# Kernel tuning notes

Measured on AMD Instinct MI355X. Metric: run time of the kernel, lower is better.

The kernel has to match this reference:

```python
import jax, jax.numpy as jnp
import numpy as np
from jax import lax

IN_CH = 256
NUM_CLASSES = 21
ROI = 7
SCALE = 1.0 / 32
SR = 2  # sampling_ratio
B = 2
NPROP = 128
FH = FW = 32
IMG = 1024
SCORE_THRESH = 0.05
NMS_THRESH = 0.5
MAX_DET = 100


def setup_inputs() -> dict:
    key = jax.random.key(0)
    ks = jax.random.split(key, 10)
    features = jax.random.normal(ks[0], (B, IN_CH, FH, FW), jnp.float32)
    x1 = jax.random.uniform(ks[1], (B, NPROP), minval=0.0, maxval=IMG - 160.0)
    y1 = jax.random.uniform(ks[2], (B, NPROP), minval=0.0, maxval=IMG - 160.0)
    w = jax.random.uniform(ks[3], (B, NPROP), minval=32.0, maxval=160.0)
    h = jax.random.uniform(ks[4], (B, NPROP), minval=32.0, maxval=160.0)
    proposals = jnp.stack([x1, y1, x1 + w, y1 + h], axis=-1)  # [B, NPROP, 4]
    img_sizes = jnp.full((B, 2), IMG, dtype=jnp.int32)  # (h, w)
    feat_dim = IN_CH * ROI * ROI

    def kaiming(k, shape):
        return jax.random.normal(k, shape, jnp.float32) * np.float32(np.sqrt(2.0 / shape[1]))

    W1 = kaiming(ks[5], (1024, feat_dim)); b1 = jnp.zeros((1024,), jnp.float32)
    W2 = kaiming(ks[6], (1024, 1024)); b2 = jnp.zeros((1024,), jnp.float32)
    Wc = jax.random.normal(ks[7], (NUM_CLASSES, 1024), jnp.float32) * 0.01
    bc = jnp.zeros((NUM_CLASSES,), jnp.float32)
    Wb = jax.random.normal(ks[8], (NUM_CLASSES * 4, 1024), jnp.float32) * 0.001
    bb = jnp.zeros((NUM_CLASSES * 4,), jnp.float32)
    return dict(features=features, proposals=proposals, img_sizes=img_sizes,
                W1=W1, b1=b1, W2=W2, b2=b2, Wc=Wc, bc=bc, Wb=Wb, bb=bb)


def roi_align(features, bidx, rois):
    """torchvision-style RoIAlign (aligned=False), spatial_scale=SCALE, sampling_ratio=SR.
    features [B,C,H,W], bidx [N] int, rois [N,4] -> [N, C*ROI*ROI] (channel-major flatten)."""
    Bf, C, H, W = features.shape
    x1 = rois[:, 0] * SCALE; y1 = rois[:, 1] * SCALE
    x2 = rois[:, 2] * SCALE; y2 = rois[:, 3] * SCALE
    rw = jnp.maximum(x2 - x1, 1.0); rh = jnp.maximum(y2 - y1, 1.0)
    bw = rw / ROI; bh = rh / ROI
    # per-bin sample offsets: [ROI, SR]
    g = jnp.arange(ROI, dtype=jnp.float32)[:, None] + (jnp.arange(SR, dtype=jnp.float32)[None, :] + 0.5) / SR
    ys = y1[:, None, None] + g[None] * bh[:, None, None]  # [N, ROI, SR]
    xs = x1[:, None, None] + g[None] * bw[:, None, None]  # [N, ROI, SR]
    y = ys[:, :, :, None, None]  # [N,ph,sy,1,1]
    x = xs[:, None, None, :, :]  # [N,1,1,pw,sx]
    inb = (y >= -1.0) & (y <= H) & (x >= -1.0) & (x <= W)  # [N,ph,sy,pw,sx]
    yc = jnp.clip(y, 0.0, H - 1.0); xc = jnp.clip(x, 0.0, W - 1.0)
    y0f = jnp.floor(yc); x0f = jnp.floor(xc)
    y0 = y0f.astype(jnp.int32); x0 = x0f.astype(jnp.int32)
    y1i = jnp.minimum(y0 + 1, H - 1); x1i = jnp.minimum(x0 + 1, W - 1)
    ly = yc - y0f; lx = xc - x0f
    hy = 1.0 - ly; hx = 1.0 - lx
    b = bidx[:, None, None, None, None]
    # gather four corners: advanced indices broadcast -> [N,ph,sy,pw,sx,C]
    f00 = features[b, :, y0, x0]
    f01 = features[b, :, y0, x1i]
    f10 = features[b, :, y1i, x0]
    f11 = features[b, :, y1i, x1i]
    val = ((hy * hx)[..., None] * f00 + (hy * lx)[..., None] * f01
           + (ly * hx)[..., None] * f10 + (ly * lx)[..., None] * f11)
    val = val * inb[..., None]
    pooled = val.mean(axis=(2, 4))            # [N, ph, pw, C]
    pooled = jnp.transpose(pooled, (0, 3, 1, 2))  # [N, C, ph, pw] (torch layout)
    return pooled.reshape(pooled.shape[0], -1)


def decode_boxes(deltas, props):
    pw = props[..., 2] - props[..., 0]
    ph = props[..., 3] - props[..., 1]
    px = props[..., 0] + pw / 2
    py = props[..., 1] + ph / 2
    cx = px + deltas[..., 0] * pw
    cy = py + deltas[..., 1] * ph
    w = pw * jnp.exp(deltas[..., 2])
    h = ph * jnp.exp(deltas[..., 3])
    return jnp.stack([cx - w / 2, cy - h / 2, cx + w / 2, cy + h / 2], axis=-1)


def nms_fixed(boxes, scores, valid, iou_thresh, max_out):
    """Greedy NMS with fixed shapes. Returns (indices[max_out], ok_mask[max_out])."""
    M = scores.shape[0]
    s = jnp.where(valid, scores, -jnp.inf)
    order = jnp.argsort(-s)
    b = boxes[order]; v = valid[order]
    bx1, by1, bx2, by2 = b[:, 0], b[:, 1], b[:, 2], b[:, 3]
    area = (bx2 - bx1) * (by2 - by1)
    idxs = jnp.arange(M)

    def body(i, keep):
        xi1 = jnp.maximum(bx1[i], bx1); yi1 = jnp.maximum(by1[i], by1)
        xi2 = jnp.minimum(bx2[i], bx2); yi2 = jnp.minimum(by2[i], by2)
        inter = jnp.maximum(xi2 - xi1, 0.0) * jnp.maximum(yi2 - yi1, 0.0)
        iou = inter / (area[i] + area - inter + 1e-9)
        suppress = (iou > iou_thresh) & (idxs > i)
        return jnp.where(keep[i], keep & ~suppress, keep)

    keep = lax.fori_loop(0, M, body, v)
    pos = jnp.where(keep, idxs, M)
    take = jnp.sort(pos)[:max_out]
    ok = take < M
    take = jnp.where(ok, take, 0)
    return order[take], ok


def postprocess_image(probs, reg, props, img_hw):
    Ncls = probs.shape[1]
    scores = probs[:, 1:]                    # [N, C-1] (skip background)
    deltas = reg[:, 1:, :]                   # [N, C-1, 4]
    boxes = decode_boxes(deltas, props[:, None, :])  # [N, C-1, 4]
    h = img_hw[0].astype(boxes.dtype); w = img_hw[1].astype(boxes.dtype)
    boxes = jnp.stack([jnp.clip(boxes[..., 0], 0.0, w), jnp.clip(boxes[..., 1], 0.0, h),
                       jnp.clip(boxes[..., 2], 0.0, w), jnp.clip(boxes[..., 3], 0.0, h)], axis=-1)
    labels = jnp.broadcast_to(jnp.arange(1, Ncls, dtype=jnp.int32)[None, :], scores.shape)
    fb = boxes.reshape(-1, 4); fs = scores.reshape(-1); fl = labels.reshape(-1)
    valid = fs > SCORE_THRESH
    maxc = jnp.max(jnp.where(valid, jnp.max(fb, axis=1), 0.0))
    off = fl.astype(fb.dtype) * (maxc + 1.0)
    zero = jnp.zeros_like(off)
    fb_off = fb + jnp.stack([off, zero, off, zero], axis=-1)
    idx, ok = nms_fixed(fb_off, fs, valid, NMS_THRESH, MAX_DET)
    m = ok.astype(fb.dtype)
    return fb[idx] * m[:, None], fs[idx] * m, fl[idx] * ok.astype(jnp.int32)


def reference(features, proposals, img_sizes, W1, b1, W2, b2, Wc, bc, Wb, bb):
    Bn, NP = proposals.shape[0], proposals.shape[1]
    bidx = jnp.repeat(jnp.arange(Bn, dtype=jnp.int32), NP)
    props_flat = proposals.reshape(-1, 4)
    roi_feats = roi_align(features, bidx, props_flat)       # [N, C*49]
    x = jax.nn.relu(roi_feats @ W1.T + b1)
    x = jax.nn.relu(x @ W2.T + b2)
    cls_logits = x @ Wc.T + bc                              # [N, NUM_CLASSES]
    box_reg = (x @ Wb.T + bb).reshape(-1, NUM_CLASSES, 4)   # [N, NUM_CLASSES, 4]
    probs = jax.nn.softmax(cls_logits, axis=-1)
    out_b, out_s, out_l = [], [], []
    for i in range(Bn):
        p = probs[i * NP:(i + 1) * NP]
        r = box_reg[i * NP:(i + 1) * NP]
        bi, si, li = postprocess_image(p, r, proposals[i], img_sizes[i])
        out_b.append(bi); out_s.append(si); out_l.append(li)
    return jnp.stack(out_b), jnp.stack(out_s), jnp.stack(out_l)
```

## Files before the change

### kernel.cpp

```cpp
#include <hip/hip_runtime.h>
#include <math.h>

#define IN_CH   256
#define NCLS    21
#define ROIW    7
#define NPROP   128
#define BATCH   2
#define NROI    (BATCH*NPROP)
#define FEAT_DIM (IN_CH*ROIW*ROIW)
#define HID     1024
#define NCAND   (NPROP*(NCLS-1))
#define MAXDET  100
#define SCORE_T 0.05f
#define NMS_T   0.5f

__global__ __launch_bounds__(256) void transpose_feat(const float* __restrict__ feat,
                                                      float* __restrict__ ft) {
    int img = blockIdx.z;
    int cb = blockIdx.y;
    int pb = blockIdx.x;
    __shared__ float t[32][33];
    int tx = threadIdx.x & 31, ty = threadIdx.x >> 5;
#pragma unroll
    for (int i = 0; i < 4; ++i) {
        int c = ty + i * 8;
        t[c][tx] = feat[(size_t)img * 262144 + (size_t)(cb * 32 + c) * 1024 + pb * 32 + tx];
    }
    __syncthreads();
#pragma unroll
    for (int i = 0; i < 4; ++i) {
        int p = ty + i * 8;
        ft[(size_t)img * 262144 + (size_t)(pb * 32 + p) * 256 + cb * 32 + tx] = t[tx][p];
    }
}

__global__ __launch_bounds__(256) void roi_align_tr(const float* __restrict__ ft,
                                                    const float* __restrict__ props,
                                                    float* __restrict__ out) {
    int n = blockIdx.x >> 1;
    int half = blockIdx.x & 1;
    int img = n / NPROP;
    int q0 = half ? 25 : 0;
    int nq = half ? 24 : 25;
    const float* pr = props + n * 4;
    float x1 = pr[0] * 0.03125f, y1 = pr[1] * 0.03125f;
    float x2 = pr[2] * 0.03125f, y2 = pr[3] * 0.03125f;
    float rw = fmaxf(x2 - x1, 1.0f), rh = fmaxf(y2 - y1, 1.0f);
    float bw = rw / 7.0f, bh = rh / 7.0f;
    int cg = threadIdx.x & 63;
    int qg = threadIdx.x >> 6;
    __shared__ float tile[25][260];
    const float* base = ft + (size_t)img * 262144 + cg * 4;
    for (int j = qg; j < nq; j += 4) {
        int q = q0 + j;
        int iy = q / 7, ix = q % 7;
        float ax = 0.f, ay = 0.f, az = 0.f, aw = 0.f;
#pragma unroll
        for (int s = 0; s < 4; ++s) {
            int sy = s >> 1, sx = s & 1;
            float gy = (float)iy + ((float)sy + 0.5f) / 2.0f;
            float gx = (float)ix + ((float)sx + 0.5f) / 2.0f;
            float y = y1 + gy * bh;
            float x = x1 + gx * bw;
            bool inb = (y >= -1.0f) && (y <= 32.0f) && (x >= -1.0f) && (x <= 32.0f);
            float yc = fminf(fmaxf(y, 0.0f), 31.0f);
            float xc = fminf(fmaxf(x, 0.0f), 31.0f);
            float y0f = floorf(yc), x0f = floorf(xc);
            int y0 = (int)y0f, x0i = (int)x0f;
            int y1i = min(y0 + 1, 31), x1i = min(x0i + 1, 31);
            float ly = yc - y0f, lx = xc - x0f;
            float hy = 1.0f - ly, hx = 1.0f - lx;
            float wg = inb ? 1.0f : 0.0f;
            float w00 = hy * hx * wg, w01 = hy * lx * wg, w10 = ly * hx * wg, w11 = ly * lx * wg;
            float4 f00 = *(const float4*)(base + (size_t)(y0 * 32 + x0i) * 256);
            float4 f01 = *(const float4*)(base + (size_t)(y0 * 32 + x1i) * 256);
            float4 f10 = *(const float4*)(base + (size_t)(y1i * 32 + x0i) * 256);
            float4 f11 = *(const float4*)(base + (size_t)(y1i * 32 + x1i) * 256);
            ax += w00 * f00.x + w01 * f01.x + w10 * f10.x + w11 * f11.x;
            ay += w00 * f00.y + w01 * f01.y + w10 * f10.y + w11 * f11.y;
            az += w00 * f00.z + w01 * f01.z + w10 * f10.z + w11 * f11.z;
            aw += w00 * f00.w + w01 * f01.w + w10 * f10.w + w11 * f11.w;
        }
        *(float4*)&tile[j][cg * 4] = make_float4(ax * 0.25f, ay * 0.25f, az * 0.25f, aw * 0.25f);
    }
    __syncthreads();
    float* ob = out + (size_t)n * FEAT_DIM + q0;
    int tid = threadIdx.x;
    if (half == 0) {
        for (int i = tid; i < 256 * 25; i += 256) {
            int c = i / 25, ql = i % 25;
            ob[c * 49 + ql] = tile[ql][c];
        }
    } else {
        for (int i = tid; i < 256 * 24; i += 256) {
            int c = i / 24, ql = i % 24;
            ob[c * 49 + ql] = tile[ql][c];
        }
    }
}

#define GBM 128
#define GBN 128
#define GBK 16
__global__ __launch_bounds__(256) void gemm_tn_part(const float* __restrict__ A,
                                                    const float* __restrict__ Wt,
                                                    float* __restrict__ Cp,
                                                    int Nr, int Mo, int K) {
    const int S = gridDim.z;
    const int kchunk = K / S;
    const int k0 = blockIdx.z * kchunk;
    const int n0 = blockIdx.y * GBM;
    const int j0 = blockIdx.x * GBN;
    __shared__ float As[GBK][GBM + 4];
    __shared__ float Ws[GBK][GBN + 4];
    const int tid = threadIdx.x;
    const int tx = tid & 15;
    const int ty = tid >> 4;
    const int r0 = tx << 2;
    const int c0 = ty << 2;
    const int srow = tid >> 1;
    const int skk = (tid & 1) << 3;
    float acc[8][8];
#pragma unroll
    for (int r = 0; r < 8; ++r)
#pragma unroll
        for (int c = 0; c < 8; ++c) acc[r][c] = 0.0f;

    const int iters = kchunk / GBK;
    const float* Abase = A + (size_t)(n0 + srow) * K + skk;
    const float* Wbase = Wt + (size_t)(j0 + srow) * K + skk;
    float4 pa0 = *(const float4*)(Abase + k0);
    float4 pa1 = *(const float4*)(Abase + k0 + 4);
    float4 pw0 = *(const float4*)(Wbase + k0);
    float4 pw1 = *(const float4*)(Wbase + k0 + 4);

#pragma unroll 1
    for (int it = 0; it < iters; ++it) {
        __syncthreads();
        As[skk + 0][srow] = pa0.x; As[skk + 1][srow] = pa0.y; As[skk + 2][srow] = pa0.z; As[skk + 3][srow] = pa0.w;
        As[skk + 4][srow] = pa1.x; As[skk + 5][srow] = pa1.y; As[skk + 6][srow] = pa1.z; As[skk + 7][srow] = pa1.w;
        Ws[skk + 0][srow] = pw0.x; Ws[skk + 1][srow] = pw0.y; Ws[skk + 2][srow] = pw0.z; Ws[skk + 3][srow] = pw0.w;
        Ws[skk + 4][srow] = pw1.x; Ws[skk + 5][srow] = pw1.y; Ws[skk + 6][srow] = pw1.z; Ws[skk + 7][srow] = pw1.w;
        __syncthreads();
        if (it + 1 < iters) {
            int kc = k0 + (it + 1) * GBK;
            pa0 = *(const float4*)(Abase + kc);
            pa1 = *(const float4*)(Abase + kc + 4);
            pw0 = *(const float4*)(Wbase + kc);
            pw1 = *(const float4*)(Wbase + kc + 4);
        }
        float4 fa0[2], fa1[2], fw0[2], fw1[2];
        fa0[0] = *(const float4*)&As[0][r0];
        fa1[0] = *(const float4*)&As[0][r0 + 64];
        fw0[0] = *(const float4*)&Ws[0][c0];
        fw1[0] = *(const float4*)&Ws[0][c0 + 64];
#pragma unroll
        for (int k = 0; k < GBK; ++k) {
            const int cur = k & 1, nxt = cur ^ 1;
            if (k + 1 < GBK) {
                fa0[nxt] = *(const float4*)&As[k + 1][r0];
                fa1[nxt] = *(const float4*)&As[k + 1][r0 + 64];
                fw0[nxt] = *(const float4*)&Ws[k + 1][c0];
                fw1[nxt] = *(const float4*)&Ws[k + 1][c0 + 64];
            }
            float a[8] = {fa0[cur].x, fa0[cur].y, fa0[cur].z, fa0[cur].w,
                          fa1[cur].x, fa1[cur].y, fa1[cur].z, fa1[cur].w};
            float w[8] = {fw0[cur].x, fw0[cur].y, fw0[cur].z, fw0[cur].w,
                          fw1[cur].x, fw1[cur].y, fw1[cur].z, fw1[cur].w};
#pragma unroll
            for (int r = 0; r < 8; ++r)
#pragma unroll
                for (int c = 0; c < 8; ++c)
                    acc[r][c] = fmaf(a[r], w[c], acc[r][c]);
        }
    }
#pragma unroll
    for (int r = 0; r < 8; ++r) {
        int gr = n0 + ((r < 4) ? (r0 + r) : (r0 + 64 + r - 4));
        float* o = Cp + ((size_t)blockIdx.z * Nr + gr) * Mo + j0;
        *(float4*)(o + c0)      = make_float4(acc[r][0], acc[r][1], acc[r][2], acc[r][3]);
        *(float4*)(o + c0 + 64) = make_float4(acc[r][4], acc[r][5], acc[r][6], acc[r][7]);
    }
}

__global__ __launch_bounds__(256) void reduce_bias_relu(const float* __restrict__ Cp,
                                                        const float* __restrict__ bias,
                                                        float* __restrict__ X,
                                                        int Nr, int Mo, int S) {
    int idx = blockIdx.x * 256 + threadIdx.x;
    int total = (Nr * Mo) >> 2;
    if (idx >= total) return;
    int e = idx << 2;
    int j = e % Mo;
    float4 s = make_float4(0.f, 0.f, 0.f, 0.f);
    for (int ss = 0; ss < S; ++ss) {
        float4 c = *(const float4*)(Cp + (size_t)ss * Nr * Mo + e);
        s.x += c.x; s.y += c.y; s.z += c.z; s.w += c.w;
    }
    float4 b = *(const float4*)(bias + j);
    s.x = fmaxf(s.x + b.x, 0.f); s.y = fmaxf(s.y + b.y, 0.f);
    s.z = fmaxf(s.z + b.z, 0.f); s.w = fmaxf(s.w + b.w, 0.f);
    *(float4*)(X + e) = s;
}

__global__ __launch_bounds__(256) void heads_cand_k(const float* __restrict__ Cp2,
                                                    const float* __restrict__ b2,
                                                    const float* __restrict__ Wc, const float* __restrict__ bc,
                                                    const float* __restrict__ Wb, const float* __restrict__ bb,
                                                    const float* __restrict__ props,
                                                    const int* __restrict__ img_sizes,
                                                    float* __restrict__ cbox,
                                                    float* __restrict__ csc,
                                                    unsigned long long* __restrict__ ckey,
                                                    int* __restrict__ vcount) {
    int n = blockIdx.x;
    int tid = threadIdx.x;
    if (n == 0 && tid < 2) vcount[tid] = 0;
    __shared__ float xs[HID];
    __shared__ float lg[NCLS];
    __shared__ float bs[84];
    __shared__ float ssum;
    {
        int e = n * HID + tid * 4;
        float4 s = make_float4(0.f, 0.f, 0.f, 0.f);
#pragma unroll
        for (int ss = 0; ss < 16; ++ss) {
            float4 c = *(const float4*)(Cp2 + (size_t)ss * (NROI * HID) + e);
            s.x += c.x; s.y += c.y; s.z += c.z; s.w += c.w;
        }
        float4 b = *(const float4*)(b2 + tid * 4);
        s.x = fmaxf(s.x + b.x, 0.f); s.y = fmaxf(s.y + b.y, 0.f);
        s.z = fmaxf(s.z + b.z, 0.f); s.w = fmaxf(s.w + b.w, 0.f);
        *(float4*)&xs[tid * 4] = s;
    }
    __syncthreads();
    int wave = tid >> 6, lane = tid & 63;
    for (int h = wave; h < 105; h += 4) {
        const float* w = (h < 21) ? (Wc + (size_t)h * HID) : (Wb + (size_t)(h - 21) * HID);
        float acc = 0.0f;
#pragma unroll
        for (int k0 = 0; k0 < HID; k0 += 256) {
            float4 wv = *(const float4*)(w + k0 + lane * 4);
            float4 xv = *(const float4*)&xs[k0 + lane * 4];
            acc = fmaf(wv.x, xv.x, acc);
            acc = fmaf(wv.y, xv.y, acc);
            acc = fmaf(wv.z, xv.z, acc);
            acc = fmaf(wv.w, xv.w, acc);
        }
#pragma unroll
        for (int m = 32; m; m >>= 1) acc += __shfl_xor(acc, m, 64);
        if (lane == 0) {
            if (h < 21) lg[h] = acc + bc[h];
            else bs[h - 21] = acc + bb[h - 21];
        }
    }
    __syncthreads();
    if (tid == 0) {
        float m = lg[0];
        for (int c = 1; c < 21; ++c) m = fmaxf(m, lg[c]);
        float s = 0.0f;
        for (int c = 0; c < 21; ++c) { float e = expf(lg[c] - m); lg[c] = e; s += e; }
        ssum = s;
    }
    __syncthreads();
    if (tid < 20) {
        int c = tid + 1;
        int img = n / NPROP;
        float s = lg[c] / ssum;
        const float* pr = props + n * 4;
        float pw = pr[2] - pr[0], ph = pr[3] - pr[1];
        float px = pr[0] + pw * 0.5f, py = pr[1] + ph * 0.5f;
        const float* d = &bs[c * 4];
        float cx = px + d[0] * pw;
        float cy = py + d[1] * ph;
        float w = pw * expf(d[2]);
        float h = ph * expf(d[3]);
        float bx1 = cx - w * 0.5f, by1 = cy - h * 0.5f, bx2 = cx + w * 0.5f, by2 = cy + h * 0.5f;
        float Wi = (float)img_sizes[img * 2 + 1], Hi = (float)img_sizes[img * 2 + 0];
        bx1 = fminf(fmaxf(bx1, 0.f), Wi); by1 = fminf(fmaxf(by1, 0.f), Hi);
        bx2 = fminf(fmaxf(bx2, 0.f), Wi); by2 = fminf(fmaxf(by2, 0.f), Hi);
        int t = n * 20 + tid;
        *(float4*)(cbox + (size_t)t * 4) = make_float4(bx1, by1, bx2, by2);
        csc[t] = s;
        bool valid = s > SCORE_T;
        unsigned int sb = __float_as_uint(s);
        int m = t - img * NCAND;
        ckey[t] = valid ? (((unsigned long long)sb << 32) | (unsigned int)(NCAND - 1 - m)) : 0ull;
    }
}

__global__ __launch_bounds__(256) void rank_k(const float* __restrict__ cbox,
                                              const float* __restrict__ csc,
                                              const unsigned long long* __restrict__ ckey,
                                              float* __restrict__ sbox, float* __restrict__ ssc,
                                              int* __restrict__ sm, int* __restrict__ vcount) {
    int img = blockIdx.x / 40;
    int seg = blockIdx.x % 40;
    int base = img * NCAND;
    int lm = threadIdx.x & 63;
    int chunk = threadIdx.x >> 6;
    int m = seg * 64 + lm;
    __shared__ __align__(16) unsigned long long keys[NCAND];
    for (int j = threadIdx.x; j < NCAND; j += 256) keys[j] = ckey[base + j];
    unsigned long long mykey = ckey[base + m];
    float s = csc[base + m];
    bool valid = s > SCORE_T;
    __syncthreads();
    const ulonglong2* kp = (const ulonglong2*)&keys[chunk * 640];
    int r = 0;
#pragma unroll 4
    for (int j = 0; j < 320; ++j) {
        ulonglong2 kk = kp[j];
        r += (kk.x > mykey) ? 1 : 0;
        r += (kk.y > mykey) ? 1 : 0;
    }
    __shared__ int part[4][64];
    part[chunk][lm] = r;
    __syncthreads();
    if (chunk == 0) {
        int rank = part[0][lm] + part[1][lm] + part[2][lm] + part[3][lm];
        if (valid) {
            int o = base + rank;
            *(float4*)(sbox + (size_t)o * 4) = *(const float4*)(cbox + (size_t)(base + m) * 4);
            ssc[o] = s;
            sm[o] = m;
        }
    }
    int cnt = __syncthreads_count((chunk == 0) && valid);
    if (threadIdx.x == 0) atomicAdd(&vcount[img], cnt);
}

__global__ __launch_bounds__(64) void nms_k(const int* __restrict__ sm,
                                            const float* __restrict__ sbox,
                                            const int* __restrict__ vcount,
                                            int* __restrict__ skeep) {
    int bid = blockIdx.x;
    int img = bid / 20;
    int cls = bid % 20 + 1;
    int V = vcount[img];
    __shared__ float lx1[128], ly1[128], lx2[128], ly2[128];
    __shared__ int lpos[128];
    __shared__ int lcnt;
    __shared__ int keepL[128];
    int lane = threadIdx.x;
    if (lane == 0) lcnt = 0;
    __syncthreads();
    for (int p0 = 0; p0 < V; p0 += 64) {
        int p = p0 + lane;
        bool pred = false;
        if (p < V) {
            int m = sm[img * NCAND + p];
            pred = (m % 20 + 1) == cls;
        }
        unsigned long long mask = __ballot(pred);
        int base = lcnt;
        if (pred) {
            int idx = base + __popcll(mask & ((1ull << lane) - 1ull));
            const float* bx = sbox + (size_t)(img * NCAND + (p0 + lane)) * 4;
            lx1[idx] = bx[0]; ly1[idx] = bx[1]; lx2[idx] = bx[2]; ly2[idx] = bx[3];
            lpos[idx] = p0 + lane;
        }
        __syncthreads();
        if (lane == 0) lcnt += (int)__popcll(mask);
        __syncthreads();
    }
    int C = lcnt;
    for (int j = lane; j < 128; j += 64) keepL[j] = 1;
    __syncthreads();
    for (int i = 0; i < C; ++i) {
        __syncthreads();
        if (keepL[i] == 0) continue;
        float X1 = lx1[i], Y1 = ly1[i], X2 = lx2[i], Y2 = ly2[i];
        float ai = (X2 - X1) * (Y2 - Y1);
        for (int j = i + 1 + lane; j < C; j += 64) {
            if (keepL[j]) {
                float xi1 = fmaxf(X1, lx1[j]);
                float yi1 = fmaxf(Y1, ly1[j]);
                float xi2 = fminf(X2, lx2[j]);
                float yi2 = fminf(Y2, ly2[j]);
                float inter = fmaxf(xi2 - xi1, 0.f) * fmaxf(yi2 - yi1, 0.f);
                float aj = (lx2[j] - lx1[j]) * (ly2[j] - ly1[j]);
                float iou = inter / (ai + aj - inter + 1e-9f);
                if (iou > NMS_T) keepL[j] = 0;
            }
        }
    }
    __syncthreads();
    for (int j = lane; j < C; j += 64) skeep[img * NCAND + lpos[j]] = keepL[j];
}

__global__ __launch_bounds__(256) void write_k(const float* __restrict__ sbox,
                                               const float* __restrict__ ssc,
                                               const int* __restrict__ sm,
                                               const int* __restrict__ skeep,
                                               const int* __restrict__ vcount,
                                               float* __restrict__ out) {
    int img = blockIdx.x;
    int tid = threadIdx.x;
    float* ob = out + img * MAXDET * 4;
    float* os = out + BATCH * MAXDET * 4 + img * MAXDET;
    float* ol = out + BATCH * MAXDET * 5 + img * MAXDET;
    for (int i = tid; i < MAXDET * 4; i += 256) ob[i] = 0.0f;
    for (int i = tid; i < MAXDET; i += 256) { os[i] = 0.0f; ol[i] = 0.0f; }
    __syncthreads();
    int V = vcount[img];
    int chunk = (V + 255) / 256;
    int lo = tid * chunk, hi = min(lo + chunk, V);
    int cnt = 0;
    for (int p = lo; p < hi; ++p) cnt += skeep[img * NCAND + p];
    __shared__ int cs[256];
    __shared__ int pre[256];
    cs[tid] = cnt;
    __syncthreads();
    if (tid == 0) {
        int run = 0;
        for (int t = 0; t < 256; ++t) { pre[t] = run; run += cs[t]; }
    }
    __syncthreads();
    int r = pre[tid];
    for (int p = lo; p < hi; ++p) {
        if (skeep[img * NCAND + p]) {
            if (r < MAXDET) {
                const float* bx = sbox + (size_t)(img * NCAND + p) * 4;
                ob[r * 4 + 0] = bx[0]; ob[r * 4 + 1] = bx[1];
                ob[r * 4 + 2] = bx[2]; ob[r * 4 + 3] = bx[3];
                os[r] = ssc[img * NCAND + p];
                ol[r] = (float)(sm[img * NCAND + p] % 20 + 1);
            }
            ++r;
        }
    }
}

extern "C" void kernel_launch(void* const* d_in, const int* in_sizes, int n_in,
                              void* d_out, int out_size, void* d_ws, size_t ws_size,
                              hipStream_t stream) {
    const float* features  = (const float*)d_in[0];
    const float* proposals = (const float*)d_in[1];
    const int*   img_sizes = (const int*)d_in[2];
    const float* W1 = (const float*)d_in[3];
    const float* b1 = (const float*)d_in[4];
    const float* W2 = (const float*)d_in[5];
    const float* b2 = (const float*)d_in[6];
    const float* Wc = (const float*)d_in[7];
    const float* bc = (const float*)d_in[8];
    const float* Wb = (const float*)d_in[9];
    const float* bb = (const float*)d_in[10];
    float* out = (float*)d_out;

    float* ws = (float*)d_ws;
    float* roi   = ws;
    float* x1    = roi + 3211264;
    float* cpart = x1 + 262144;
    float* featT = cpart;
    float* cbox  = cpart + 16 * 262144;
    float* csc   = cbox + 20480;
    unsigned long long* ckey = (unsigned long long*)(csc + 5120);
    float* sbox  = csc + 5120 + 10240;
    float* ssc   = sbox + 20480;
    int*   sm    = (int*)(ssc + 5120);
    int*   skeep = sm + 5120;
    int*   vcnt  = skeep + 5120;

    hipLaunchKernelGGL(transpose_feat, dim3(32, 8, 2), dim3(256), 0, stream, features, featT);
    hipLaunchKernelGGL(roi_align_tr, dim3(NROI * 2), dim3(256), 0, stream, featT, proposals, roi);
    hipLaunchKernelGGL(gemm_tn_part, dim3(8, 2, 16), dim3(256), 0, stream, roi, W1, cpart, NROI, HID, FEAT_DIM);
    hipLaunchKernelGGL(reduce_bias_relu, dim3(256), dim3(256), 0, stream, cpart, b1, x1, NROI, HID, 16);
    hipLaunchKernelGGL(gemm_tn_part, dim3(8, 2, 16), dim3(256), 0, stream, x1, W2, cpart, NROI, HID, HID);
    hipLaunchKernelGGL(heads_cand_k, dim3(NROI), dim3(256), 0, stream, cpart, b2, Wc, bc, Wb, bb,
                       proposals, img_sizes, cbox, csc, ckey, vcnt);
    hipLaunchKernelGGL(rank_k, dim3(80), dim3(256), 0, stream, cbox, csc, ckey, sbox, ssc, sm, vcnt);
    hipLaunchKernelGGL(nms_k, dim3(BATCH * 20), dim3(64), 0, stream, sm, sbox, vcnt, skeep);
    hipLaunchKernelGGL(write_k, dim3(BATCH), dim3(256), 0, stream, sbox, ssc, sm, skeep, vcnt, out);
}
```

Baseline: 319.9 us.

## Fuse detection tail into one cooperative kernel and simplify GEMM LDS loads

Merges the heads/candidate, ranking, NMS and output-writing kernels into a single cooperative kernel separated by grid-wide syncs. This removes several kernel launches and inter-kernel gaps in the post-processing tail. NMS now runs with 256 threads per block instead of 64. Separately, the GEMM inner loop drops its register double-buffering of shared-memory fragments in favour of direct per-k loads, which may reduce register pressure but loses the explicit load/compute overlap. Cooperative launch adds grid-sync overhead and requires all blocks to be co-resident.

```diff
diff --git a/kernel.cpp b/kernel.cpp
--- a/kernel.cpp
+++ b/kernel.cpp
@@ -1,5 +1,8 @@
 #include <hip/hip_runtime.h>
+#include <hip/hip_cooperative_groups.h>
 #include <math.h>
+
+namespace cg = cooperative_groups;
 
 #define IN_CH   256
 #define NCLS    21
@@ -149,24 +152,14 @@
             pw0 = *(const float4*)(Wbase + kc);
             pw1 = *(const float4*)(Wbase + kc + 4);
         }
-        float4 fa0[2], fa1[2], fw0[2], fw1[2];
-        fa0[0] = *(const float4*)&As[0][r0];
-        fa1[0] = *(const float4*)&As[0][r0 + 64];
-        fw0[0] = *(const float4*)&Ws[0][c0];
-        fw1[0] = *(const float4*)&Ws[0][c0 + 64];
 #pragma unroll
         for (int k = 0; k < GBK; ++k) {
-            const int cur = k & 1, nxt = cur ^ 1;
-            if (k + 1 < GBK) {
-                fa0[nxt] = *(const float4*)&As[k + 1][r0];
-                fa1[nxt] = *(const float4*)&As[k + 1][r0 + 64];
-                fw0[nxt] = *(const float4*)&Ws[k + 1][c0];
-                fw1[nxt] = *(const float4*)&Ws[k + 1][c0 + 64];
-            }
-            float a[8] = {fa0[cur].x, fa0[cur].y, fa0[cur].z, fa0[cur].w,
-                          fa1[cur].x, fa1[cur].y, fa1[cur].z, fa1[cur].w};
-            float w[8] = {fw0[cur].x, fw0[cur].y, fw0[cur].z, fw0[cur].w,
-                          fw1[cur].x, fw1[cur].y, fw1[cur].z, fw1[cur].w};
+            float4 t0 = *(const float4*)&As[k][r0];
+            float4 t1 = *(const float4*)&As[k][r0 + 64];
+            float4 u0 = *(const float4*)&Ws[k][c0];
+            float4 u1 = *(const float4*)&Ws[k][c0 + 64];
+            float a[8] = {t0.x, t0.y, t0.z, t0.w, t1.x, t1.y, t1.z, t1.w};
+            float w[8] = {u0.x, u0.y, u0.z, u0.w, u1.x, u1.y, u1.z, u1.w};
 #pragma unroll
             for (int r = 0; r < 8; ++r)
 #pragma unroll
@@ -203,231 +196,224 @@
     *(float4*)(X + e) = s;
 }
 
-__global__ __launch_bounds__(256) void heads_cand_k(const float* __restrict__ Cp2,
-                                                    const float* __restrict__ b2,
-                                                    const float* __restrict__ Wc, const float* __restrict__ bc,
-                                                    const float* __restrict__ Wb, const float* __restrict__ bb,
-                                                    const float* __restrict__ props,
-                                                    const int* __restrict__ img_sizes,
-                                                    float* __restrict__ cbox,
-                                                    float* __restrict__ csc,
-                                                    unsigned long long* __restrict__ ckey,
-                                                    int* __restrict__ vcount) {
-    int n = blockIdx.x;
-    int tid = threadIdx.x;
-    if (n == 0 && tid < 2) vcount[tid] = 0;
+__global__ __launch_bounds__(256) void tail_k(const float* __restrict__ Cp2,
+                                              const float* __restrict__ b2,
+                                              const float* __restrict__ Wc, const float* __restrict__ bc,
+                                              const float* __restrict__ Wb, const float* __restrict__ bb,
+                                              const float* __restrict__ props,
+                                              const int* __restrict__ img_sizes,
+                                              float* __restrict__ cbox,
+                                              float* __restrict__ csc,
+                                              unsigned long long* __restrict__ ckey,
+                                              float* __restrict__ sbox, float* __restrict__ ssc,
+                                              int* __restrict__ sm, int* __restrict__ skeep,
+                                              int* __restrict__ vcount,
+                                              float* __restrict__ out) {
+    cg::grid_group grid = cg::this_grid();
+    const int bid = blockIdx.x;
+    const int tid = threadIdx.x;
+
     __shared__ float xs[HID];
     __shared__ float lg[NCLS];
     __shared__ float bs[84];
     __shared__ float ssum;
-    {
-        int e = n * HID + tid * 4;
-        float4 s = make_float4(0.f, 0.f, 0.f, 0.f);
-#pragma unroll
-        for (int ss = 0; ss < 16; ++ss) {
-            float4 c = *(const float4*)(Cp2 + (size_t)ss * (NROI * HID) + e);
-            s.x += c.x; s.y += c.y; s.z += c.z; s.w += c.w;
-        }
-        float4 b = *(const float4*)(b2 + tid * 4);
-        s.x = fmaxf(s.x + b.x, 0.f); s.y = fmaxf(s.y + b.y, 0.f);
-        s.z = fmaxf(s.z + b.z, 0.f); s.w = fmaxf(s.w + b.w, 0.f);
-        *(float4*)&xs[tid * 4] = s;
-    }
-    __syncthreads();
-    int wave = tid >> 6, lane = tid & 63;
-    for (int h = wave; h < 105; h += 4) {
-        const float* w = (h < 21) ? (Wc + (size_t)h * HID) : (Wb + (size_t)(h - 21) * HID);
-        float acc = 0.0f;
-#pragma unroll
-        for (int k0 = 0; k0 < HID; k0 += 256) {
-            float4 wv = *(const float4*)(w + k0 + lane * 4);
-            float4 xv = *(const float4*)&xs[k0 + lane * 4];
-            acc = fmaf(wv.x, xv.x, acc);
-            acc = fmaf(wv.y, xv.y, acc);
-            acc = fmaf(wv.z, xv.z, acc);
-            acc = fmaf(wv.w, xv.w, acc);
-        }
-#pragma unroll
-        for (int m = 32; m; m >>= 1) acc += __shfl_xor(acc, m, 64);
-        if (lane == 0) {
-            if (h < 21) lg[h] = acc + bc[h];
-            else bs[h - 21] = acc + bb[h - 21];
-        }
-    }
-    __syncthreads();
-    if (tid == 0) {
-        float m = lg[0];
-        for (int c = 1; c < 21; ++c) m = fmaxf(m, lg[c]);
-        float s = 0.0f;
-        for (int c = 0; c < 21; ++c) { float e = expf(lg[c] - m); lg[c] = e; s += e; }
-        ssum = s;
-    }
-    __syncthreads();
-    if (tid < 20) {
-        int c = tid + 1;
-        int img = n / NPROP;
-        float s = lg[c] / ssum;
-        const float* pr = props + n * 4;
-        float pw = pr[2] - pr[0], ph = pr[3] - pr[1];
-        float px = pr[0] + pw * 0.5f, py = pr[1] + ph * 0.5f;
-        const float* d = &bs[c * 4];
-        float cx = px + d[0] * pw;
-        float cy = py + d[1] * ph;
-        float w = pw * expf(d[2]);
-        float h = ph * expf(d[3]);
-        float bx1 = cx - w * 0.5f, by1 = cy - h * 0.5f, bx2 = cx + w * 0.5f, by2 = cy + h * 0.5f;
-        float Wi = (float)img_sizes[img * 2 + 1], Hi = (float)img_sizes[img * 2 + 0];
-        bx1 = fminf(fmaxf(bx1, 0.f), Wi); by1 = fminf(fmaxf(by1, 0.f), Hi);
-        bx2 = fminf(fmaxf(bx2, 0.f), Wi); by2 = fminf(fmaxf(by2, 0.f), Hi);
-        int t = n * 20 + tid;
-        *(float4*)(cbox + (size_t)t * 4) = make_float4(bx1, by1, bx2, by2);
-        csc[t] = s;
-        bool valid = s > SCORE_T;
-        unsigned int sb = __float_as_uint(s);
-        int m = t - img * NCAND;
-        ckey[t] = valid ? (((unsigned long long)sb << 32) | (unsigned int)(NCAND - 1 - m)) : 0ull;
-    }
-}
-
-__global__ __launch_bounds__(256) void rank_k(const float* __restrict__ cbox,
-                                              const float* __restrict__ csc,
-                                              const unsigned long long* __restrict__ ckey,
-                                              float* __restrict__ sbox, float* __restrict__ ssc,
-                                              int* __restrict__ sm, int* __restrict__ vcount) {
-    int img = blockIdx.x / 40;
-    int seg = blockIdx.x % 40;
-    int base = img * NCAND;
-    int lm = threadIdx.x & 63;
-    int chunk = threadIdx.x >> 6;
-    int m = seg * 64 + lm;
     __shared__ __align__(16) unsigned long long keys[NCAND];
-    for (int j = threadIdx.x; j < NCAND; j += 256) keys[j] = ckey[base + j];
-    unsigned long long mykey = ckey[base + m];
-    float s = csc[base + m];
-    bool valid = s > SCORE_T;
-    __syncthreads();
-    const ulonglong2* kp = (const ulonglong2*)&keys[chunk * 640];
-    int r = 0;
-#pragma unroll 4
-    for (int j = 0; j < 320; ++j) {
-        ulonglong2 kk = kp[j];
-        r += (kk.x > mykey) ? 1 : 0;
-        r += (kk.y > mykey) ? 1 : 0;
-    }
     __shared__ int part[4][64];
-    part[chunk][lm] = r;
-    __syncthreads();
-    if (chunk == 0) {
-        int rank = part[0][lm] + part[1][lm] + part[2][lm] + part[3][lm];
-        if (valid) {
-            int o = base + rank;
-            *(float4*)(sbox + (size_t)o * 4) = *(const float4*)(cbox + (size_t)(base + m) * 4);
-            ssc[o] = s;
-            sm[o] = m;
-        }
-    }
-    int cnt = __syncthreads_count((chunk == 0) && valid);
-    if (threadIdx.x == 0) atomicAdd(&vcount[img], cnt);
-}
-
-__global__ __launch_bounds__(64) void nms_k(const int* __restrict__ sm,
-                                            const float* __restrict__ sbox,
-                                            const int* __restrict__ vcount,
-                                            int* __restrict__ skeep) {
-    int bid = blockIdx.x;
-    int img = bid / 20;
-    int cls = bid % 20 + 1;
-    int V = vcount[img];
     __shared__ float lx1[128], ly1[128], lx2[128], ly2[128];
     __shared__ int lpos[128];
     __shared__ int lcnt;
     __shared__ int keepL[128];
-    int lane = threadIdx.x;
-    if (lane == 0) lcnt = 0;
-    __syncthreads();
-    for (int p0 = 0; p0 < V; p0 += 64) {
-        int p = p0 + lane;
-        bool pred = false;
-        if (p < V) {
-            int m = sm[img * NCAND + p];
-            pred = (m % 20 + 1) == cls;
-        }
-        unsigned long long mask = __ballot(pred);
-        int base = lcnt;
-        if (pred) {
-            int idx = base + __popcll(mask & ((1ull << lane) - 1ull));
-            const float* bx = sbox + (size_t)(img * NCAND + (p0 + lane)) * 4;
-            lx1[idx] = bx[0]; ly1[idx] = bx[1]; lx2[idx] = bx[2]; ly2[idx] = bx[3];
-            lpos[idx] = p0 + lane;
-        }
-        __syncthreads();
-        if (lane == 0) lcnt += (int)__popcll(mask);
-        __syncthreads();
-    }
-    int C = lcnt;
-    for (int j = lane; j < 128; j += 64) keepL[j] = 1;
-    __syncthreads();
-    for (int i = 0; i < C; ++i) {
-        __syncthreads();
-        if (keepL[i] == 0) continue;
-        float X1 = lx1[i], Y1 = ly1[i], X2 = lx2[i], Y2 = ly2[i];
-        float ai = (X2 - X1) * (Y2 - Y1);
-        for (int j = i + 1 + lane; j < C; j += 64) {
-            if (keepL[j]) {
-                float xi1 = fmaxf(X1, lx1[j]);
-                float yi1 = fmaxf(Y1, ly1[j]);
-                float xi2 = fminf(X2, lx2[j]);
-                float yi2 = fminf(Y2, ly2[j]);
-                float inter = fmaxf(xi2 - xi1, 0.f) * fmaxf(yi2 - yi1, 0.f);
-                float aj = (lx2[j] - lx1[j]) * (ly2[j] - ly1[j]);
-                float iou = inter / (ai + aj - inter + 1e-9f);
-                if (iou > NMS_T) keepL[j] = 0;
-            }
-        }
-    }
-    __syncthreads();
-    for (int j = lane; j < C; j += 64) skeep[img * NCAND + lpos[j]] = keepL[j];
-}
-
-__global__ __launch_bounds__(256) void write_k(const float* __restrict__ sbox,
-                                               const float* __restrict__ ssc,
-                                               const int* __restrict__ sm,
-                                               const int* __restrict__ skeep,
-                                               const int* __restrict__ vcount,
-                                               float* __restrict__ out) {
-    int img = blockIdx.x;
-    int tid = threadIdx.x;
-    float* ob = out + img * MAXDET * 4;
-    float* os = out + BATCH * MAXDET * 4 + img * MAXDET;
-    float* ol = out + BATCH * MAXDET * 5 + img * MAXDET;
-    for (int i = tid; i < MAXDET * 4; i += 256) ob[i] = 0.0f;
-    for (int i = tid; i < MAXDET; i += 256) { os[i] = 0.0f; ol[i] = 0.0f; }
-    __syncthreads();
-    int V = vcount[img];
-    int chunk = (V + 255) / 256;
-    int lo = tid * chunk, hi = min(lo + chunk, V);
-    int cnt = 0;
-    for (int p = lo; p < hi; ++p) cnt += skeep[img * NCAND + p];
     __shared__ int cs[256];
     __shared__ int pre[256];
-    cs[tid] = cnt;
-    __syncthreads();
-    if (tid == 0) {
-        int run = 0;
-        for (int t = 0; t < 256; ++t) { pre[t] = run; run += cs[t]; }
-    }
-    __syncthreads();
-    int r = pre[tid];
-    for (int p = lo; p < hi; ++p) {
-        if (skeep[img * NCAND + p]) {
-            if (r < MAXDET) {
+
+    {
+        int n = bid;
+        if (n == 0 && tid < 2) vcount[tid] = 0;
+        {
+            int e = n * HID + tid * 4;
+            float4 s = make_float4(0.f, 0.f, 0.f, 0.f);
+#pragma unroll
+            for (int ss = 0; ss < 16; ++ss) {
+                float4 c = *(const float4*)(Cp2 + (size_t)ss * (NROI * HID) + e);
+                s.x += c.x; s.y += c.y; s.z += c.z; s.w += c.w;
+            }
+            float4 b = *(const float4*)(b2 + tid * 4);
+            s.x = fmaxf(s.x + b.x, 0.f); s.y = fmaxf(s.y + b.y, 0.f);
+            s.z = fmaxf(s.z + b.z, 0.f); s.w = fmaxf(s.w + b.w, 0.f);
+            *(float4*)&xs[tid * 4] = s;
+        }
+        __syncthreads();
+        int wave = tid >> 6, lane = tid & 63;
+        for (int h = wave; h < 105; h += 4) {
+            const float* w = (h < 21) ? (Wc + (size_t)h * HID) : (Wb + (size_t)(h - 21) * HID);
+            float acc = 0.0f;
+#pragma unroll
+            for (int k0 = 0; k0 < HID; k0 += 256) {
+                float4 wv = *(const float4*)(w + k0 + lane * 4);
+                float4 xv = *(const float4*)&xs[k0 + lane * 4];
+                acc = fmaf(wv.x, xv.x, acc);
+                acc = fmaf(wv.y, xv.y, acc);
+                acc = fmaf(wv.z, xv.z, acc);
+                acc = fmaf(wv.w, xv.w, acc);
+            }
+#pragma unroll
+            for (int m = 32; m; m >>= 1) acc += __shfl_xor(acc, m, 64);
+            if (lane == 0) {
+                if (h < 21) lg[h] = acc + bc[h];
+                else bs[h - 21] = acc + bb[h - 21];
+            }
+        }
+        __syncthreads();
+        if (tid == 0) {
+            float m = lg[0];
+            for (int c = 1; c < 21; ++c) m = fmaxf(m, lg[c]);
+            float s = 0.0f;
+            for (int c = 0; c < 21; ++c) { float e = expf(lg[c] - m); lg[c] = e; s += e; }
+            ssum = s;
+        }
+        __syncthreads();
+        if (tid < 20) {
+            int c = tid + 1;
+            int img = n / NPROP;
+            float s = lg[c] / ssum;
+            const float* pr = props + n * 4;
+            float pw = pr[2] - pr[0], ph = pr[3] - pr[1];
+            float px = pr[0] + pw * 0.5f, py = pr[1] + ph * 0.5f;
+            const float* d = &bs[c * 4];
+            float cx = px + d[0] * pw;
+            float cy = py + d[1] * ph;
+            float w = pw * expf(d[2]);
+            float h = ph * expf(d[3]);
+            float bx1 = cx - w * 0.5f, by1 = cy - h * 0.5f, bx2 = cx + w * 0.5f, by2 = cy + h * 0.5f;
+            float Wi = (float)img_sizes[img * 2 + 1], Hi = (float)img_sizes[img * 2 + 0];
+            bx1 = fminf(fmaxf(bx1, 0.f), Wi); by1 = fminf(fmaxf(by1, 0.f), Hi);
+            bx2 = fminf(fmaxf(bx2, 0.f), Wi); by2 = fminf(fmaxf(by2, 0.f), Hi);
+            int t = n * 20 + tid;
+            *(float4*)(cbox + (size_t)t * 4) = make_float4(bx1, by1, bx2, by2);
+            csc[t] = s;
+            bool valid = s > SCORE_T;
+            unsigned int sb = __float_as_uint(s);
+            int m = t - img * NCAND;
+            ckey[t] = valid ? (((unsigned long long)sb << 32) | (unsigned int)(NCAND - 1 - m)) : 0ull;
+        }
+    }
+    grid.sync();
+
+    if (bid < 80) {
+        int img = bid / 40;
+        int seg = bid % 40;
+        int base = img * NCAND;
+        int lm = tid & 63;
+        int chunk = tid >> 6;
+        int m = seg * 64 + lm;
+        for (int j = tid; j < NCAND; j += 256) keys[j] = ckey[base + j];
+        unsigned long long mykey = ckey[base + m];
+        float s = csc[base + m];
+        bool valid = s > SCORE_T;
+        __syncthreads();
+        const ulonglong2* kp = (const ulonglong2*)&keys[chunk * 640];
+        int r = 0;
+#pragma unroll 4
+        for (int j = 0; j < 320; ++j) {
+            ulonglong2 kk = kp[j];
+            r += (kk.x > mykey) ? 1 : 0;
+            r += (kk.y > mykey) ? 1 : 0;
+        }
+        part[chunk][lm] = r;
+        __syncthreads();
+        if (chunk == 0) {
+            int rank = part[0][lm] + part[1][lm] + part[2][lm] + part[3][lm];
+            if (valid) {
+                int o = base + rank;
+                *(float4*)(sbox + (size_t)o * 4) = *(const float4*)(cbox + (size_t)(base + m) * 4);
+                ssc[o] = s;
+                sm[o] = m;
+            }
+        }
+        int cnt = __syncthreads_count((chunk == 0) && valid);
+        if (tid == 0) atomicAdd(&vcount[img], cnt);
+    }
+    grid.sync();
+
+    if (bid < 40) {
+        int img = bid / 20;
+        int cls = bid % 20 + 1;
+        int V = vcount[img];
+        if (tid == 0) lcnt = 0;
+        __syncthreads();
+        for (int p0 = 0; p0 < V; p0 += 64) {
+            int p = p0 + tid;
+            bool pred = (tid < 64) && (p < V) && ((sm[img * NCAND + p] % 20 + 1) == cls);
+            unsigned long long mask = __ballot(pred);
+            int base = lcnt;
+            if (pred) {
+                int idx = base + (int)__popcll(mask & ((1ull << tid) - 1ull));
                 const float* bx = sbox + (size_t)(img * NCAND + p) * 4;
-                ob[r * 4 + 0] = bx[0]; ob[r * 4 + 1] = bx[1];
-                ob[r * 4 + 2] = bx[2]; ob[r * 4 + 3] = bx[3];
-                os[r] = ssc[img * NCAND + p];
-                ol[r] = (float)(sm[img * NCAND + p] % 20 + 1);
-            }
-            ++r;
+                lx1[idx] = bx[0]; ly1[idx] = bx[1]; lx2[idx] = bx[2]; ly2[idx] = bx[3];
+                lpos[idx] = p;
+            }
+            __syncthreads();
+            if (tid == 0) lcnt += (int)__popcll(mask);
+            __syncthreads();
+        }
+        int C = lcnt;
+        for (int j = tid; j < 128; j += 256) keepL[j] = 1;
+        __syncthreads();
+        for (int i = 0; i < C; ++i) {
+            __syncthreads();
+            if (keepL[i] == 0) continue;
+            float X1 = lx1[i], Y1 = ly1[i], X2 = lx2[i], Y2 = ly2[i];
+            float ai = (X2 - X1) * (Y2 - Y1);
+            for (int j = i + 1 + tid; j < C; j += 256) {
+                if (keepL[j]) {
+                    float xi1 = fmaxf(X1, lx1[j]);
+                    float yi1 = fmaxf(Y1, ly1[j]);
+                    float xi2 = fminf(X2, lx2[j]);
+                    float yi2 = fminf(Y2, ly2[j]);
+                    float inter = fmaxf(xi2 - xi1, 0.f) * fmaxf(yi2 - yi1, 0.f);
+                    float aj = (lx2[j] - lx1[j]) * (ly2[j] - ly1[j]);
+                    float iou = inter / (ai + aj - inter + 1e-9f);
+                    if (iou > NMS_T) keepL[j] = 0;
+                }
+            }
+        }
+        __syncthreads();
+        for (int j = tid; j < C; j += 256) skeep[img * NCAND + lpos[j]] = keepL[j];
+    }
+    grid.sync();
+
+    if (bid < BATCH) {
+        int img = bid;
+        float* ob = out + img * MAXDET * 4;
+        float* os = out + BATCH * MAXDET * 4 + img * MAXDET;
+        float* ol = out + BATCH * MAXDET * 5 + img * MAXDET;
+        for (int i = tid; i < MAXDET * 4; i += 256) ob[i] = 0.0f;
+        for (int i = tid; i < MAXDET; i += 256) { os[i] = 0.0f; ol[i] = 0.0f; }
+        __syncthreads();
+        int V = vcount[img];
+        int chunk = (V + 255) / 256;
+        int lo = tid * chunk, hi = min(lo + chunk, V);
+        int cnt = 0;
+        for (int p = lo; p < hi; ++p) cnt += skeep[img * NCAND + p];
+        cs[tid] = cnt;
+        __syncthreads();
+        if (tid == 0) {
+            int run = 0;
+            for (int t = 0; t < 256; ++t) { pre[t] = run; run += cs[t]; }
+        }
+        __syncthreads();
+        int r = pre[tid];
+        for (int p = lo; p < hi; ++p) {
+            if (skeep[img * NCAND + p]) {
+                if (r < MAXDET) {
+                    const float* bx = sbox + (size_t)(img * NCAND + p) * 4;
+                    ob[r * 4 + 0] = bx[0]; ob[r * 4 + 1] = bx[1];
+                    ob[r * 4 + 2] = bx[2]; ob[r * 4 + 3] = bx[3];
+                    os[r] = ssc[img * NCAND + p];
+                    ol[r] = (float)(sm[img * NCAND + p] % 20 + 1);
+                }
+                ++r;
+            }
         }
     }
 }
@@ -467,9 +453,14 @@
     hipLaunchKernelGGL(gemm_tn_part, dim3(8, 2, 16), dim3(256), 0, stream, roi, W1, cpart, NROI, HID, FEAT_DIM);
     hipLaunchKernelGGL(reduce_bias_relu, dim3(256), dim3(256), 0, stream, cpart, b1, x1, NROI, HID, 16);
     hipLaunchKernelGGL(gemm_tn_part, dim3(8, 2, 16), dim3(256), 0, stream, x1, W2, cpart, NROI, HID, HID);
-    hipLaunchKernelGGL(heads_cand_k, dim3(NROI), dim3(256), 0, stream, cpart, b2, Wc, bc, Wb, bb,
-                       proposals, img_sizes, cbox, csc, ckey, vcnt);
-    hipLaunchKernelGGL(rank_k, dim3(80), dim3(256), 0, stream, cbox, csc, ckey, sbox, ssc, sm, vcnt);
-    hipLaunchKernelGGL(nms_k, dim3(BATCH * 20), dim3(64), 0, stream, sm, sbox, vcnt, skeep);
-    hipLaunchKernelGGL(write_k, dim3(BATCH), dim3(256), 0, stream, sbox, ssc, sm, skeep, vcnt, out);
-}
+    {
+        void* args[] = {
+            (void*)&cpart, (void*)&b2, (void*)&Wc, (void*)&bc, (void*)&Wb, (void*)&bb,
+            (void*)&proposals, (void*)&img_sizes,
+            (void*)&cbox, (void*)&csc, (void*)&ckey,
+            (void*)&sbox, (void*)&ssc, (void*)&sm, (void*)&skeep, (void*)&vcnt,
+            (void*)&out
+        };
+        hipLaunchCooperativeKernel((const void*)tail_k, dim3(NROI), dim3(256), args, 0, stream);
+    }
+}
```

Measured after the change: 396.0 us. 1.24x slower.
